# Kernel optimization log

Hardware: AMD Instinct MI355X
Metric: run time of the kernel (lower is better)

Reference implementation:

```python
import jax, jax.numpy as jnp
import numpy as np

B, C, H, W = 64, 1, 1024, 1024
KS, F, OUT = 16, 128, 10
L = (H // KS) * (W // KS)  # 4096 non-overlapping patch locations


def setup_inputs() -> dict:
    key = jax.random.key(0)
    k1, k2, k3, k4, k5 = jax.random.split(key, 5)
    x = jax.random.normal(k1, (B, C, H, W), dtype=jnp.float32)
    weight = jax.random.normal(k2, (F, L, C, KS, KS), dtype=jnp.float32)
    bias = jax.random.normal(k3, (F, L, C), dtype=jnp.float32)
    dec_w = jax.random.normal(k4, (OUT, F * L * C), dtype=jnp.float32) * 0.01
    dec_b = jax.random.normal(k5, (OUT,), dtype=jnp.float32)
    return {"x": x, "weight": weight, "bias": bias, "dec_w": dec_w, "dec_b": dec_b}


def reference(x, weight, bias, dec_w, dec_b):
    b, c, h, w = x.shape
    f, l, cw, kh, kw = weight.shape
    # Non-overlapping unfold (stride == kernel): [B,C,H,W] -> [B, L, C, kh, kw]
    patches = x.reshape(b, c, h // kh, kh, w // kw, kw)
    patches = patches.transpose(0, 2, 4, 1, 3, 5).reshape(b, l, c, kh, kw)
    # Locally-connected multiply-sum: out[b,f,l,c] = sum_ij patches[b,l,c,i,j] * weight[f,l,c,i,j]
    y = jnp.einsum('blcij,flcij->bflc', patches, weight) + bias
    y = jax.nn.relu(y)
    y = y.reshape(b, -1)  # [B, F*L*C], f-major like torch's view
    return y @ dec_w.T + dec_b
```

## Files before the change

### kernel.cpp

```cpp
#include <hip/hip_runtime.h>
#include <hip/hip_bf16.h>

#define B_    64
#define F_    128
#define L_    4096
#define K_    256
#define OUT_  10
#define HW_   (1024 * 1024)
#define WIMG_ 1024

typedef __attribute__((ext_vector_type(8))) short bf16x8;
typedef __attribute__((ext_vector_type(4))) float f32x4;

static __device__ __forceinline__ unsigned short f2bf(float f) {
    return __builtin_bit_cast(unsigned short, __float2bfloat16(f));
}

__global__ __launch_bounds__(512)
void lcn_main(const float* __restrict__ x, const float* __restrict__ wgt,
              const float* __restrict__ bias, const float* __restrict__ dec_w,
              float* __restrict__ ws) {
    const int l  = blockIdx.x;
    const int hb = l >> 6, wb = l & 63;
    const int t  = threadIdx.x;
    const int lane = t & 63;
    const int wid  = t >> 6;
    const int ln15 = lane & 15;
    const int kg   = lane >> 4;
    const int wm2  = wid >> 2;
    const int wf   = wid & 3;

    __shared__ union {
        struct { unsigned short xs[B_ * K_]; unsigned short wm[F_ * 128]; } s;
        float ysm[B_][132];
        float red[16][B_][OUT_];
    } u;

    {
        const int xrow = lane >> 2, xc4 = (lane & 3) * 4;
        const float* xb = x + (size_t)(hb * 16 + xrow) * WIMG_ + wb * 16 + xc4;
        #pragma unroll
        for (int i = 0; i < 8; ++i) {
            const int b = wid * 8 + i;
            float4 v = *reinterpret_cast<const float4*>(xb + (size_t)b * HW_);
            const int k = xrow * 16 + xc4;
            *reinterpret_cast<ushort4*>(&u.s.xs[b * K_ + (k ^ ((b & 7) << 3))]) =
                make_ushort4(f2bf(v.x), f2bf(v.y), f2bf(v.z), f2bf(v.w));
        }
    }

    f32x4 acc[2][2];
    #pragma unroll
    for (int m = 0; m < 2; ++m)
        #pragma unroll
        for (int n = 0; n < 2; ++n)
            acc[m][n] = (f32x4){0.f, 0.f, 0.f, 0.f};

    const int wsf_ = wid * 16 + (lane >> 5);
    const int wk4  = (lane & 31) * 4;
    #pragma unroll
    for (int p = 0; p < 2; ++p) {
        if (p) __syncthreads();
        #pragma unroll
        for (int i = 0; i < 8; ++i) {
            const int f = wsf_ + i * 2;
            float4 v = *reinterpret_cast<const float4*>(
                wgt + ((size_t)f * L_ + l) * K_ + p * 128 + wk4);
            *reinterpret_cast<ushort4*>(&u.s.wm[f * 128 + (wk4 ^ ((f & 7) << 3))]) =
                make_ushort4(f2bf(v.x), f2bf(v.y), f2bf(v.z), f2bf(v.w));
        }
        __syncthreads();

        #pragma unroll
        for (int ks = 0; ks < 4; ++ks) {
            const int kloc = ks * 32 + kg * 8;
            bf16x8 a[2], bb[2];
            #pragma unroll
            for (int m = 0; m < 2; ++m) {
                const int b = wm2 * 32 + m * 16 + ln15;
                a[m] = *reinterpret_cast<const bf16x8*>(
                    &u.s.xs[b * K_ + ((p * 128 + kloc) ^ ((b & 7) << 3))]);
            }
            #pragma unroll
            for (int n = 0; n < 2; ++n) {
                const int f = wf * 32 + n * 16 + ln15;
                bb[n] = *reinterpret_cast<const bf16x8*>(
                    &u.s.wm[f * 128 + (kloc ^ ((f & 7) << 3))]);
            }
            #pragma unroll
            for (int m = 0; m < 2; ++m)
                #pragma unroll
                for (int n = 0; n < 2; ++n)
                    acc[m][n] = __builtin_amdgcn_mfma_f32_16x16x32_bf16(
                        a[m], bb[n], acc[m][n], 0, 0, 0);
        }
    }

    float bv[2];
    #pragma unroll
    for (int n = 0; n < 2; ++n)
        bv[n] = bias[(size_t)(wf * 32 + n * 16 + ln15) * L_ + l];

    __syncthreads();

    #pragma unroll
    for (int m = 0; m < 2; ++m)
        #pragma unroll
        for (int n = 0; n < 2; ++n)
            #pragma unroll
            for (int r = 0; r < 4; ++r) {
                const int b = wm2 * 32 + m * 16 + kg * 4 + r;
                const int f = wf * 32 + n * 16 + ln15;
                u.ysm[b][f] = fmaxf(acc[m][n][r] + bv[n], 0.f);
            }
    __syncthreads();

    const int tt = t & 255;
    const int oh = t >> 8;
    const int tx = tt & 15, ty = tt >> 4;
    const int b0 = tx * 4, f0 = ty * 8;

    float yv[4][8];
    #pragma unroll
    for (int bi = 0; bi < 4; ++bi) {
        f32x4 p0 = *reinterpret_cast<const f32x4*>(&u.ysm[b0 + bi][f0]);
        f32x4 p1 = *reinterpret_cast<const f32x4*>(&u.ysm[b0 + bi][f0 + 4]);
        yv[bi][0] = p0.x; yv[bi][1] = p0.y; yv[bi][2] = p0.z; yv[bi][3] = p0.w;
        yv[bi][4] = p1.x; yv[bi][5] = p1.y; yv[bi][6] = p1.z; yv[bi][7] = p1.w;
    }
    __syncthreads();

    float part[4][5];
    #pragma unroll
    for (int bi = 0; bi < 4; ++bi)
        #pragma unroll
        for (int oo = 0; oo < 5; ++oo) part[bi][oo] = 0.f;

    #pragma unroll
    for (int fj = 0; fj < 8; ++fj) {
        #pragma unroll
        for (int oo = 0; oo < 5; ++oo) {
            const int o = oh * 5 + oo;
            const float dw = dec_w[(size_t)o * ((size_t)F_ * L_) + (size_t)(f0 + fj) * L_ + l];
            #pragma unroll
            for (int bi = 0; bi < 4; ++bi)
                part[bi][oo] = fmaf(yv[bi][fj], dw, part[bi][oo]);
        }
    }

    #pragma unroll
    for (int bi = 0; bi < 4; ++bi)
        #pragma unroll
        for (int oo = 0; oo < 5; ++oo)
            u.red[ty][b0 + bi][oh * 5 + oo] = part[bi][oo];
    __syncthreads();

    for (int idx = t; idx < B_ * OUT_; idx += 512) {
        const int b = idx / OUT_;
        const int o = idx - b * OUT_;
        float s = 0.f;
        #pragma unroll
        for (int g = 0; g < 16; ++g) s += u.red[g][b][o];
        ws[(size_t)b * ((size_t)L_ * OUT_) + (size_t)l * OUT_ + o] = s;
    }
}

__global__ __launch_bounds__(640)
void lcn_reduce(const float* __restrict__ ws, const float* __restrict__ dec_b,
                float* __restrict__ out) {
    const int b = blockIdx.x;
    const int j = threadIdx.x;
    const float* base = ws + (size_t)b * ((size_t)L_ * OUT_);

    float s = 0.f;
    #pragma unroll 8
    for (int i = 0; i < 64; ++i)
        s += base[j + i * (64 * OUT_)];

    __shared__ float lds[64 * OUT_];
    lds[j] = s;
    __syncthreads();

    if (j < OUT_) {
        float tot = dec_b[j];
        #pragma unroll
        for (int lc = 0; lc < 64; ++lc) tot += lds[lc * OUT_ + j];
        out[b * OUT_ + j] = tot;
    }
}

extern "C" void kernel_launch(void* const* d_in, const int* in_sizes, int n_in,
                              void* d_out, int out_size, void* d_ws, size_t ws_size,
                              hipStream_t stream) {
    const float* x     = (const float*)d_in[0];
    const float* wgt   = (const float*)d_in[1];
    const float* bias  = (const float*)d_in[2];
    const float* dec_w = (const float*)d_in[3];
    const float* dec_b = (const float*)d_in[4];
    float* out = (float*)d_out;
    float* wsf = (float*)d_ws;

    lcn_main<<<dim3(L_), dim3(512), 0, stream>>>(x, wgt, bias, dec_w, wsf);
    lcn_reduce<<<dim3(B_), dim3(640), 0, stream>>>(wsf, dec_b, out);
}
```

Measured before the change: 236.0 us.

## Split x staging into K halves and prefetch second weight half into registers

The x patch staging buffer in LDS is halved by loading only the half of the K dimension currently in use. The second half of the weights is prefetched into registers while the first half is computed, so global loads overlap with MFMA work. Launch bounds now request 6 waves per SIMD to raise occupancy using the smaller LDS footprint. The cost is extra registers for the prefetched weights and an extra barrier pair between the halves.

```diff
diff --git a/kernel.cpp b/kernel.cpp
--- a/kernel.cpp
+++ b/kernel.cpp
@@ -16,7 +16,7 @@
     return __builtin_bit_cast(unsigned short, __float2bfloat16(f));
 }
 
-__global__ __launch_bounds__(512)
+__global__ __launch_bounds__(512, 6)
 void lcn_main(const float* __restrict__ x, const float* __restrict__ wgt,
               const float* __restrict__ bias, const float* __restrict__ dec_w,
               float* __restrict__ ws) {
@@ -31,23 +31,48 @@
     const int wf   = wid & 3;
 
     __shared__ union {
-        struct { unsigned short xs[B_ * K_]; unsigned short wm[F_ * 128]; } s;
+        struct { unsigned short xs[B_ * 128]; unsigned short wm[F_ * 128]; } s;
         float ysm[B_][132];
         float red[16][B_][OUT_];
     } u;
 
-    {
-        const int xrow = lane >> 2, xc4 = (lane & 3) * 4;
-        const float* xb = x + (size_t)(hb * 16 + xrow) * WIMG_ + wb * 16 + xc4;
+    const int sb  = (t >> 2) & 63;
+    const int sc4 = t & 3;
+    const int srh = t >> 8;
+    const float* xbase = x + (size_t)sb * HW_ + (size_t)(hb * 16) * WIMG_
+                           + wb * 16 + sc4 * 4;
+    const int sswz = (sb & 7) << 3;
+    auto XSTAGE = [&](int kh) {
+        #pragma unroll
+        for (int i = 0; i < 4; ++i) {
+            const int r = kh * 8 + srh * 4 + i;
+            float4 v = *reinterpret_cast<const float4*>(xbase + (size_t)r * WIMG_);
+            const int kloc = (srh * 4 + i) * 16 + sc4 * 4;
+            *reinterpret_cast<ushort4*>(&u.s.xs[sb * 128 + (kloc ^ sswz)]) =
+                make_ushort4(f2bf(v.x), f2bf(v.y), f2bf(v.z), f2bf(v.w));
+        }
+    };
+
+    const int wsf_ = wid * 16 + (lane >> 5);
+    const int wk4  = (lane & 31) * 4;
+    float4 wg[8];
+    auto WLOAD = [&](int kh) {
         #pragma unroll
         for (int i = 0; i < 8; ++i) {
-            const int b = wid * 8 + i;
-            float4 v = *reinterpret_cast<const float4*>(xb + (size_t)b * HW_);
-            const int k = xrow * 16 + xc4;
-            *reinterpret_cast<ushort4*>(&u.s.xs[b * K_ + (k ^ ((b & 7) << 3))]) =
-                make_ushort4(f2bf(v.x), f2bf(v.y), f2bf(v.z), f2bf(v.w));
-        }
-    }
+            const int f = wsf_ + i * 2;
+            wg[i] = *reinterpret_cast<const float4*>(
+                wgt + ((size_t)f * L_ + l) * K_ + kh * 128 + wk4);
+        }
+    };
+    auto WSTORE = [&]() {
+        #pragma unroll
+        for (int i = 0; i < 8; ++i) {
+            const int f = wsf_ + i * 2;
+            *reinterpret_cast<ushort4*>(
+                &u.s.wm[f * 128 + (wk4 ^ ((f & 7) << 3))]) =
+                make_ushort4(f2bf(wg[i].x), f2bf(wg[i].y), f2bf(wg[i].z), f2bf(wg[i].w));
+        }
+    };
 
     f32x4 acc[2][2];
     #pragma unroll
@@ -56,21 +81,14 @@
         for (int n = 0; n < 2; ++n)
             acc[m][n] = (f32x4){0.f, 0.f, 0.f, 0.f};
 
-    const int wsf_ = wid * 16 + (lane >> 5);
-    const int wk4  = (lane & 31) * 4;
-    #pragma unroll
-    for (int p = 0; p < 2; ++p) {
-        if (p) __syncthreads();
-        #pragma unroll
-        for (int i = 0; i < 8; ++i) {
-            const int f = wsf_ + i * 2;
-            float4 v = *reinterpret_cast<const float4*>(
-                wgt + ((size_t)f * L_ + l) * K_ + p * 128 + wk4);
-            *reinterpret_cast<ushort4*>(&u.s.wm[f * 128 + (wk4 ^ ((f & 7) << 3))]) =
-                make_ushort4(f2bf(v.x), f2bf(v.y), f2bf(v.z), f2bf(v.w));
-        }
-        __syncthreads();
-
+    WLOAD(0);
+    XSTAGE(0);
+    WSTORE();
+    WLOAD(1);
+    __syncthreads();
+
+    #pragma unroll
+    for (int kh = 0; kh < 2; ++kh) {
         #pragma unroll
         for (int ks = 0; ks < 4; ++ks) {
             const int kloc = ks * 32 + kg * 8;
@@ -79,7 +97,7 @@
             for (int m = 0; m < 2; ++m) {
                 const int b = wm2 * 32 + m * 16 + ln15;
                 a[m] = *reinterpret_cast<const bf16x8*>(
-                    &u.s.xs[b * K_ + ((p * 128 + kloc) ^ ((b & 7) << 3))]);
+                    &u.s.xs[b * 128 + (kloc ^ ((b & 7) << 3))]);
             }
             #pragma unroll
             for (int n = 0; n < 2; ++n) {
@@ -94,6 +112,12 @@
                     acc[m][n] = __builtin_amdgcn_mfma_f32_16x16x32_bf16(
                         a[m], bb[n], acc[m][n], 0, 0, 0);
         }
+        if (kh == 0) {
+            __syncthreads();
+            XSTAGE(1);
+            WSTORE();
+            __syncthreads();
+        }
     }
 
     float bv[2];
@@ -161,7 +185,7 @@
         float s = 0.f;
         #pragma unroll
         for (int g = 0; g < 16; ++g) s += u.red[g][b][o];
-        ws[(size_t)b * ((size_t)L_ * OUT_) + (size_t)l * OUT_ + o] = s;
+        ws[((size_t)b * L_ + l) * OUT_ + o] = s;
     }
 }
 
@@ -177,7 +201,7 @@
     for (int i = 0; i < 64; ++i)
         s += base[j + i * (64 * OUT_)];
 
-    __shared__ float lds[64 * OUT_];
+    __shared__ float lds[640];
     lds[j] = s;
     __syncthreads();
 
```

Result: slower. 328.6 us (+39.2%).

## Shrink main kernel to 256 threads with K-split x staging and simpler decoder

Applied to the files above, without the earlier changes.

The main kernel now uses 256 threads (4 waves), each computing a 32x64 tile with 2x4 MFMAs. The x patch is staged in two K halves alongside the weights, which halves the LDS footprint, and launch bounds request 4 blocks per CU to raise occupancy. The decoder stage is simplified: 160 threads each loop over all 128 features, reading y from LDS, so the cross-group reduction buffer and its extra barriers are gone. The trade-off is fewer threads per block doing the global loads, more register pressure per thread, and a serial 128-step decoder loop on a subset of threads.

```diff
diff --git a/kernel.cpp b/kernel.cpp
--- a/kernel.cpp
+++ b/kernel.cpp
@@ -16,7 +16,7 @@
     return __builtin_bit_cast(unsigned short, __float2bfloat16(f));
 }
 
-__global__ __launch_bounds__(512)
+__global__ __launch_bounds__(256, 4)
 void lcn_main(const float* __restrict__ x, const float* __restrict__ wgt,
               const float* __restrict__ bias, const float* __restrict__ dec_w,
               float* __restrict__ ws) {
@@ -27,141 +27,115 @@
     const int wid  = t >> 6;
     const int ln15 = lane & 15;
     const int kg   = lane >> 4;
-    const int wm2  = wid >> 2;
-    const int wf   = wid & 3;
+    const int m2   = wid >> 1;
+    const int n2   = wid & 1;
 
     __shared__ union {
-        struct { unsigned short xs[B_ * K_]; unsigned short wm[F_ * 128]; } s;
+        struct { unsigned short xs[B_ * 128]; unsigned short wm[F_ * 128]; } s;
         float ysm[B_][132];
-        float red[16][B_][OUT_];
     } u;
 
-    {
-        const int xrow = lane >> 2, xc4 = (lane & 3) * 4;
-        const float* xb = x + (size_t)(hb * 16 + xrow) * WIMG_ + wb * 16 + xc4;
+    const int lane32 = lane & 31;
+    const int fhi    = lane >> 5;
+    auto WSTAGE = [&](int kh) {
         #pragma unroll
-        for (int i = 0; i < 8; ++i) {
-            const int b = wid * 8 + i;
-            float4 v = *reinterpret_cast<const float4*>(xb + (size_t)b * HW_);
-            const int k = xrow * 16 + xc4;
-            *reinterpret_cast<ushort4*>(&u.s.xs[b * K_ + (k ^ ((b & 7) << 3))]) =
+        for (int i = 0; i < 16; ++i) {
+            const int f = wid * 32 + i * 2 + fhi;
+            float4 v = *reinterpret_cast<const float4*>(
+                wgt + ((size_t)f * L_ + l) * K_ + kh * 128 + lane32 * 4);
+            *reinterpret_cast<ushort4*>(
+                &u.s.wm[f * 128 + ((lane32 * 4) ^ ((f & 7) << 3))]) =
                 make_ushort4(f2bf(v.x), f2bf(v.y), f2bf(v.z), f2bf(v.w));
         }
-    }
+    };
 
-    f32x4 acc[2][2];
+    const int sb  = t >> 2;
+    const int scq = t & 3;
+    const float* xbase = x + (size_t)sb * HW_ + (size_t)(hb * 16) * WIMG_
+                           + wb * 16 + scq * 4;
+    const int sswz = (sb & 7) << 3;
+    auto XSTAGE = [&](int kh) {
+        #pragma unroll
+        for (int r = 0; r < 8; ++r) {
+            float4 v = *reinterpret_cast<const float4*>(
+                xbase + (size_t)(kh * 8 + r) * WIMG_);
+            const int kloc = r * 16 + scq * 4;
+            *reinterpret_cast<ushort4*>(&u.s.xs[sb * 128 + (kloc ^ sswz)]) =
+                make_ushort4(f2bf(v.x), f2bf(v.y), f2bf(v.z), f2bf(v.w));
+        }
+    };
+
+    float bv[4];
+    #pragma unroll
+    for (int n = 0; n < 4; ++n)
+        bv[n] = bias[(size_t)(n2 * 64 + n * 16 + ln15) * L_ + l];
+
+    f32x4 acc[2][4];
     #pragma unroll
     for (int m = 0; m < 2; ++m)
         #pragma unroll
-        for (int n = 0; n < 2; ++n)
+        for (int n = 0; n < 4; ++n)
             acc[m][n] = (f32x4){0.f, 0.f, 0.f, 0.f};
 
-    const int wsf_ = wid * 16 + (lane >> 5);
-    const int wk4  = (lane & 31) * 4;
     #pragma unroll
-    for (int p = 0; p < 2; ++p) {
-        if (p) __syncthreads();
-        #pragma unroll
-        for (int i = 0; i < 8; ++i) {
-            const int f = wsf_ + i * 2;
-            float4 v = *reinterpret_cast<const float4*>(
-                wgt + ((size_t)f * L_ + l) * K_ + p * 128 + wk4);
-            *reinterpret_cast<ushort4*>(&u.s.wm[f * 128 + (wk4 ^ ((f & 7) << 3))]) =
-                make_ushort4(f2bf(v.x), f2bf(v.y), f2bf(v.z), f2bf(v.w));
-        }
+    for (int kh = 0; kh < 2; ++kh) {
+        WSTAGE(kh);
+        XSTAGE(kh);
         __syncthreads();
 
         #pragma unroll
         for (int ks = 0; ks < 4; ++ks) {
             const int kloc = ks * 32 + kg * 8;
-            bf16x8 a[2], bb[2];
+            bf16x8 a[2], bb[4];
             #pragma unroll
             for (int m = 0; m < 2; ++m) {
-                const int b = wm2 * 32 + m * 16 + ln15;
+                const int b = m2 * 32 + m * 16 + ln15;
                 a[m] = *reinterpret_cast<const bf16x8*>(
-                    &u.s.xs[b * K_ + ((p * 128 + kloc) ^ ((b & 7) << 3))]);
+                    &u.s.xs[b * 128 + (kloc ^ ((b & 7) << 3))]);
             }
             #pragma unroll
-            for (int n = 0; n < 2; ++n) {
-                const int f = wf * 32 + n * 16 + ln15;
+            for (int n = 0; n < 4; ++n) {
+                const int f = n2 * 64 + n * 16 + ln15;
                 bb[n] = *reinterpret_cast<const bf16x8*>(
                     &u.s.wm[f * 128 + (kloc ^ ((f & 7) << 3))]);
             }
             #pragma unroll
             for (int m = 0; m < 2; ++m)
                 #pragma unroll
-                for (int n = 0; n < 2; ++n)
+                for (int n = 0; n < 4; ++n)
                     acc[m][n] = __builtin_amdgcn_mfma_f32_16x16x32_bf16(
                         a[m], bb[n], acc[m][n], 0, 0, 0);
         }
+        __syncthreads();
     }
-
-    float bv[2];
-    #pragma unroll
-    for (int n = 0; n < 2; ++n)
-        bv[n] = bias[(size_t)(wf * 32 + n * 16 + ln15) * L_ + l];
-
-    __syncthreads();
 
     #pragma unroll
     for (int m = 0; m < 2; ++m)
         #pragma unroll
-        for (int n = 0; n < 2; ++n)
+        for (int n = 0; n < 4; ++n)
             #pragma unroll
             for (int r = 0; r < 4; ++r) {
-                const int b = wm2 * 32 + m * 16 + kg * 4 + r;
-                const int f = wf * 32 + n * 16 + ln15;
+                const int b = m2 * 32 + m * 16 + kg * 4 + r;
+                const int f = n2 * 64 + n * 16 + ln15;
                 u.ysm[b][f] = fmaxf(acc[m][n][r] + bv[n], 0.f);
             }
     __syncthreads();
 
-    const int tt = t & 255;
-    const int oh = t >> 8;
-    const int tx = tt & 15, ty = tt >> 4;
-    const int b0 = tx * 4, f0 = ty * 8;
-
-    float yv[4][8];
-    #pragma unroll
-    for (int bi = 0; bi < 4; ++bi) {
-        f32x4 p0 = *reinterpret_cast<const f32x4*>(&u.ysm[b0 + bi][f0]);
-        f32x4 p1 = *reinterpret_cast<const f32x4*>(&u.ysm[b0 + bi][f0 + 4]);
-        yv[bi][0] = p0.x; yv[bi][1] = p0.y; yv[bi][2] = p0.z; yv[bi][3] = p0.w;
-        yv[bi][4] = p1.x; yv[bi][5] = p1.y; yv[bi][6] = p1.z; yv[bi][7] = p1.w;
-    }
-    __syncthreads();
-
-    float part[4][5];
-    #pragma unroll
-    for (int bi = 0; bi < 4; ++bi)
-        #pragma unroll
-        for (int oo = 0; oo < 5; ++oo) part[bi][oo] = 0.f;
-
-    #pragma unroll
-    for (int fj = 0; fj < 8; ++fj) {
-        #pragma unroll
-        for (int oo = 0; oo < 5; ++oo) {
-            const int o = oh * 5 + oo;
-            const float dw = dec_w[(size_t)o * ((size_t)F_ * L_) + (size_t)(f0 + fj) * L_ + l];
+    if (t < 16 * OUT_) {
+        const int tx = t & 15;
+        const int o  = t >> 4;
+        float part[4] = {0.f, 0.f, 0.f, 0.f};
+        const float* dwp = dec_w + (size_t)o * ((size_t)F_ * L_) + l;
+        #pragma unroll 8
+        for (int f = 0; f < F_; ++f) {
+            const float dw = dwp[(size_t)f * L_];
             #pragma unroll
             for (int bi = 0; bi < 4; ++bi)
-                part[bi][oo] = fmaf(yv[bi][fj], dw, part[bi][oo]);
+                part[bi] = fmaf(u.ysm[tx + bi * 16][f], dw, part[bi]);
         }
-    }
-
-    #pragma unroll
-    for (int bi = 0; bi < 4; ++bi)
         #pragma unroll
-        for (int oo = 0; oo < 5; ++oo)
-            u.red[ty][b0 + bi][oh * 5 + oo] = part[bi][oo];
-    __syncthreads();
-
-    for (int idx = t; idx < B_ * OUT_; idx += 512) {
-        const int b = idx / OUT_;
-        const int o = idx - b * OUT_;
-        float s = 0.f;
-        #pragma unroll
-        for (int g = 0; g < 16; ++g) s += u.red[g][b][o];
-        ws[(size_t)b * ((size_t)L_ * OUT_) + (size_t)l * OUT_ + o] = s;
+        for (int bi = 0; bi < 4; ++bi)
+            ws[((size_t)(tx + bi * 16) * L_ + l) * OUT_ + o] = part[bi];
     }
 }
 
@@ -177,7 +151,7 @@
     for (int i = 0; i < 64; ++i)
         s += base[j + i * (64 * OUT_)];
 
-    __shared__ float lds[64 * OUT_];
+    __shared__ float lds[640];
     lds[j] = s;
     __syncthreads();
 
@@ -200,6 +174,6 @@
     float* out = (float*)d_out;
     float* wsf = (float*)d_ws;
 
-    lcn_main<<<dim3(L_), dim3(512), 0, stream>>>(x, wgt, bias, dec_w, wsf);
+    lcn_main<<<dim3(L_), dim3(256), 0, stream>>>(x, wgt, bias, dec_w, wsf);
     lcn_reduce<<<dim3(B_), dim3(640), 0, stream>>>(wsf, dec_b, out);
 }
```

After: 265.0 us. 12.3% more time.
